# Optimization experiments

Measured on AMD Instinct MI355X. Metric: run time of the kernel, lower is better.

Reference implementation:

```python
import jax, jax.numpy as jnp
import numpy as np


def _forward(f2e_emb, score_mat, rel_features, Wk, bk,
             batch_heads, batch_rels, batch_tails, edge_mat, eps):
    B, N, D = f2e_emb.shape
    R = rel_features.shape[0]
    dt = f2e_emb.dtype
    # -cdist(x, x) then row softmax (F.softmax dim=1 on a 2D mat == last axis)
    x2 = jnp.sum(f2e_emb * f2e_emb, axis=-1)                              # [B,N]
    d2 = x2[:, :, None] + x2[:, None, :] - 2.0 * jnp.einsum('bnd,bmd->bnm', f2e_emb, f2e_emb)
    sim = jax.nn.softmax(-jnp.sqrt(jnp.maximum(d2, 0.0)), axis=-1)        # [B,N,N]
    prob = jnp.einsum('bnk,bmk->bnm', sim, score_mat)                     # sim @ score_mat.T
    cand = (prob > eps) & (edge_mat < 1)                                  # candidate (row,col) pairs
    # torch.multinomial(sim[row], 1) per candidate pair -> gumbel-max categorical,
    # one independent draw per (b, row, col) over the row's similarity distribution
    logits = jnp.log(sim)[:, :, None, :]                                  # [B,N,1,N]
    s = jax.random.categorical(jax.random.key(42),
                               jax.lax.stop_gradient(jnp.broadcast_to(logits, (B, N, N, N))),
                               axis=-1)                                    # [B,N,N]
    b3 = jnp.arange(B)[:, None, None]
    r3 = jnp.arange(N)[None, :, None]
    c3 = jnp.arange(N)[None, None, :]
    new_rel = edge_mat[b3, s, c3]                                          # [B,N,N]
    valid = (cand & (new_rel != 0)).astype(dt)
    # per-(node, relation) incidence counts: exactly equivalent to the
    # fact2head_mat/fact2tail_mat sparse.mm aggregation of kb_self_linear(rel_features[rel])
    counts = jnp.zeros((B * N * R,), dt)
    counts = counts.at[((b3 * N + r3) * R + new_rel).ravel()].add(valid.ravel())  # new edge -> head
    counts = counts.at[((b3 * N + c3) * R + new_rel).ravel()].add(valid.ravel())  # new edge -> tail
    b2 = jnp.arange(B)[:, None]
    ones = jnp.ones(batch_heads.shape, dt)
    counts = counts.at[((b2 * N + batch_heads) * R + batch_rels).ravel()].add(ones.ravel())
    counts = counts.at[((b2 * N + batch_tails) * R + batch_rels).ravel()].add(ones.ravel())
    counts = counts.reshape(B, N, R)
    Wr = rel_features @ Wk + bk                                            # kb_self_linear(rel_features) [R,O]
    return jax.nn.relu(jnp.einsum('bnr,ro->bno', counts, Wr))              # [B,N,O]


def setup_inputs():
    key = jax.random.key(0)
    ks = jax.random.split(key, 10)
    B, N, D, O, R, E = 8, 256, 256, 256, 512, 8192
    return {
        'f2e_emb': jax.random.normal(ks[0], (B, N, D), jnp.float32),
        'score_mat': jax.random.normal(ks[1], (B, N, N), jnp.float32),
        'rel_features': jax.random.normal(ks[2], (R, D), jnp.float32),
        'Wk': jax.random.normal(ks[3], (D, O), jnp.float32) / np.sqrt(D).astype(np.float32),
        'bk': jnp.zeros((O,), jnp.float32),
        'local_entity': jax.random.randint(ks[4], (B, N), 0, N, jnp.int32),
        'batch_heads': jax.random.randint(ks[5], (B, E), 0, N, jnp.int32),
        'batch_rels': jax.random.randint(ks[6], (B, E), 0, R, jnp.int32),
        'batch_tails': jax.random.randint(ks[7], (B, E), 0, N, jnp.int32),
        'edge_mat': jax.random.randint(ks[8], (B, N, N), 0, 4, jnp.int32),
        'eps': 0,
    }


def reference(f2e_emb, score_mat, rel_features, Wk, bk, local_entity,
              batch_heads, batch_rels, batch_tails, edge_mat, eps):
    return _forward(f2e_emb, score_mat, rel_features, Wk, bk,
                    batch_heads, batch_rels, batch_tails, edge_mat, eps)
```

## Files before the change

kernel.cpp:

```cpp
#include <hip/hip_runtime.h>
#include <stdint.h>

#define B 8
#define N 256
#define D 256
#define O 256
#define R 512
#define E 8192
#define TR 4
#define F32_TINY 1.17549435e-38f

__device__ __forceinline__ void threefry2x32_k42(uint32_t x0, uint32_t x1,
                                                 uint32_t& o0, uint32_t& o1) {
  const uint32_t ks0 = 0u;
  const uint32_t ks1 = 42u;
  const uint32_t ks2 = 0u ^ 42u ^ 0x1BD11BDAu;
  x0 += ks0; x1 += ks1;
#define TF_R(r) { x0 += x1; x1 = (x1 << (r)) | (x1 >> (32 - (r))); x1 ^= x0; }
  TF_R(13) TF_R(15) TF_R(26) TF_R(6)
  x0 += ks1; x1 += ks2 + 1u;
  TF_R(17) TF_R(29) TF_R(16) TF_R(24)
  x0 += ks2; x1 += ks0 + 2u;
  TF_R(13) TF_R(15) TF_R(26) TF_R(6)
  x0 += ks0; x1 += ks1 + 3u;
  TF_R(17) TF_R(29) TF_R(16) TF_R(24)
  x0 += ks1; x1 += ks2 + 4u;
  TF_R(13) TF_R(15) TF_R(26) TF_R(6)
  x0 += ks2; x1 += ks0 + 5u;
#undef TF_R
  o0 = x0; o1 = x1;
}

__device__ __forceinline__ float gumbel_from_bits_f(float f) {
  float u = (f == 0.0f) ? F32_TINY : f;
  return -logf(-logf(u));
}

__global__ __launch_bounds__(256) void transpose_kernel(const float* __restrict__ score,
                                                        float* __restrict__ scoreT,
                                                        const float* __restrict__ f2e,
                                                        float* __restrict__ f2eT) {
  __shared__ float tile[64][65];
  int blk = blockIdx.x;
  const float* src = (blk < 128) ? score : f2e;
  float* dst = (blk < 128) ? scoreT : f2eT;
  int b7 = blk & 127;
  int bb = b7 >> 4, t = b7 & 15, ti = t >> 2, tj = t & 3;
  size_t base = (size_t)bb * 65536;
  int c = threadIdx.x & 63, r4 = threadIdx.x >> 6;
#pragma unroll
  for (int rr = 0; rr < 64; rr += 4) {
    int row = rr + r4;
    tile[row][c] = src[base + (size_t)(ti * 64 + row) * 256 + tj * 64 + c];
  }
  __syncthreads();
#pragma unroll
  for (int rr = 0; rr < 64; rr += 4) {
    int row = rr + r4;
    dst[base + (size_t)(tj * 64 + row) * 256 + ti * 64 + c] = tile[c][row];
  }
}

__global__ __launch_bounds__(256) void x2_kernel(const float* __restrict__ f2e,
                                                 float* __restrict__ x2) {
  int i = blockIdx.x * 256 + threadIdx.x;
  const float4* p = (const float4*)(f2e + (size_t)i * D);
  double s = 0.0;
  for (int d = 0; d < D / 4; ++d) {
    float4 v = p[d];
    s += (double)v.x * v.x; s += (double)v.y * v.y;
    s += (double)v.z * v.z; s += (double)v.w * v.w;
  }
  x2[i] = (float)s;
}

__global__ __launch_bounds__(256) void wr_kernel(const float* __restrict__ relf,
                                                 const float* __restrict__ Wk,
                                                 const float* __restrict__ bk,
                                                 float* __restrict__ Wr) {
  int r0 = blockIdx.x * TR;
  int o = threadIdx.x;
  __shared__ float rrow[TR][D];
#pragma unroll
  for (int r = 0; r < TR; ++r) rrow[r][o] = relf[(size_t)(r0 + r) * D + o];
  __syncthreads();
  double acc[TR] = {0, 0, 0, 0};
  for (int d = 0; d < D; d += 4) {
    float w0 = Wk[(size_t)(d + 0) * O + o];
    float w1 = Wk[(size_t)(d + 1) * O + o];
    float w2 = Wk[(size_t)(d + 2) * O + o];
    float w3 = Wk[(size_t)(d + 3) * O + o];
#pragma unroll
    for (int r = 0; r < TR; ++r) {
      float4 a = *(const float4*)&rrow[r][d];
      acc[r] += (double)a.x * w0; acc[r] += (double)a.y * w1;
      acc[r] += (double)a.z * w2; acc[r] += (double)a.w * w3;
    }
  }
  float bv = bk[o];
#pragma unroll
  for (int r = 0; r < TR; ++r) Wr[(size_t)(r0 + r) * O + o] = (float)acc[r] + bv;
}

__global__ __launch_bounds__(256) void sim_kernel(const float* __restrict__ f2e,
                                                  const float* __restrict__ f2eT,
                                                  const float* __restrict__ x2,
                                                  float* __restrict__ sim,
                                                  float* __restrict__ logits,
                                                  float* __restrict__ laux) {
  int bn0 = blockIdx.x * TR;
  int b = bn0 >> 8;
  int tid = threadIdx.x, lane = tid & 63, w = tid >> 6;
  __shared__ float arow[TR][256];
  __shared__ float nbuf[TR][256];
#pragma unroll
  for (int r = 0; r < TR; ++r) arow[r][tid] = f2e[(size_t)(bn0 + r) * 256 + tid];
  __syncthreads();
  double acc[TR] = {0, 0, 0, 0};
  const float* fT = f2eT + (size_t)b * 65536 + tid;
  for (int dd = 0; dd < 256; dd += 4) {
    float b0 = fT[(size_t)(dd + 0) * 256];
    float b1 = fT[(size_t)(dd + 1) * 256];
    float b2 = fT[(size_t)(dd + 2) * 256];
    float b3 = fT[(size_t)(dd + 3) * 256];
#pragma unroll
    for (int r = 0; r < TR; ++r) {
      float4 a = *(const float4*)&arow[r][dd];
      acc[r] += (double)a.x * b0; acc[r] += (double)a.y * b1;
      acc[r] += (double)a.z * b2; acc[r] += (double)a.w * b3;
    }
  }
  float x2c = x2[b * 256 + tid];
#pragma unroll
  for (int r = 0; r < TR; ++r) {
    float d2 = (x2[bn0 + r] + x2c) - 2.0f * (float)acc[r];
    nbuf[r][tid] = -sqrtf(fmaxf(d2, 0.0f));
  }
  __syncthreads();
  float v0 = nbuf[w][lane], v1 = nbuf[w][lane + 64],
        v2 = nbuf[w][lane + 128], v3 = nbuf[w][lane + 192];
  float mx = fmaxf(fmaxf(v0, v1), fmaxf(v2, v3));
#pragma unroll
  for (int off = 32; off > 0; off >>= 1) mx = fmaxf(mx, __shfl_xor(mx, off));
  float p0 = expf(v0 - mx), p1 = expf(v1 - mx), p2 = expf(v2 - mx), p3 = expf(v3 - mx);
  double sd = (double)p0 + (double)p1 + (double)p2 + (double)p3;
#pragma unroll
  for (int off = 32; off > 0; off >>= 1) sd += __shfl_xor(sd, off);
  float denom = (float)sd;
  float s0 = p0 / denom, s1 = p1 / denom, s2 = p2 / denom, s3 = p3 / denom;
  size_t rb = (size_t)(bn0 + w) * 256;
  sim[rb + lane] = s0; sim[rb + lane + 64] = s1;
  sim[rb + lane + 128] = s2; sim[rb + lane + 192] = s3;
  float l0 = logf(s0), l1 = logf(s1), l2 = logf(s2), l3 = logf(s3);
  logits[rb + lane] = l0; logits[rb + lane + 64] = l1;
  logits[rb + lane + 128] = l2; logits[rb + lane + 192] = l3;
  int dm = (bn0 + w) & 255;
  int dj = dm >> 6, dl = dm & 63;
  float e0 = (dj == 0 && lane == dl) ? -3.4e38f : l0;
  float e1 = (dj == 1 && lane == dl) ? -3.4e38f : l1;
  float e2 = (dj == 2 && lane == dl) ? -3.4e38f : l2;
  float e3 = (dj == 3 && lane == dl) ? -3.4e38f : l3;
  float Lm = fmaxf(fmaxf(e0, e1), fmaxf(e2, e3));
#pragma unroll
  for (int off = 32; off > 0; off >>= 1) Lm = fmaxf(Lm, __shfl_xor(Lm, off));
  float lown = (dj == 0) ? l0 : (dj == 1) ? l1 : (dj == 2) ? l2 : l3;
  float l_n = __shfl(lown, dl);
  if (lane == 0) {
    laux[2 * (bn0 + w) + 0] = l_n;
    laux[2 * (bn0 + w) + 1] = Lm;
  }
}

__global__ __launch_bounds__(256) void cand_kernel(const float* __restrict__ sim,
                                                   const float* __restrict__ scoreT,
                                                   const int* __restrict__ edge,
                                                   const int* __restrict__ epsp,
                                                   unsigned char* __restrict__ cand) {
  int bn0 = blockIdx.x * TR;
  int b = bn0 >> 8;
  int tid = threadIdx.x;
  __shared__ float srow[TR][256];
#pragma unroll
  for (int r = 0; r < TR; ++r) srow[r][tid] = sim[(size_t)(bn0 + r) * 256 + tid];
  __syncthreads();
  double acc[TR] = {0, 0, 0, 0};
  const float* sT = scoreT + (size_t)b * 65536 + tid;
  for (int kk = 0; kk < 256; kk += 4) {
    float b0 = sT[(size_t)(kk + 0) * 256];
    float b1 = sT[(size_t)(kk + 1) * 256];
    float b2 = sT[(size_t)(kk + 2) * 256];
    float b3 = sT[(size_t)(kk + 3) * 256];
#pragma unroll
    for (int r = 0; r < TR; ++r) {
      float4 a = *(const float4*)&srow[r][kk];
      acc[r] += (double)a.x * b0; acc[r] += (double)a.y * b1;
      acc[r] += (double)a.z * b2; acc[r] += (double)a.w * b3;
    }
  }
  float epsv = (float)epsp[0];
#pragma unroll
  for (int r = 0; r < TR; ++r) {
    int em = edge[(size_t)(bn0 + r) * 256 + tid];
    cand[(size_t)(bn0 + r) * 256 + tid] =
        ((float)acc[r] > epsv && em < 1) ? 1 : 0;
  }
}

__global__ __launch_bounds__(256) void sample_kernel(const float* __restrict__ logits,
                                                     const float* __restrict__ laux,
                                                     const unsigned char* __restrict__ cand,
                                                     const int* __restrict__ edge,
                                                     float* __restrict__ counts) {
  int wid = threadIdx.x >> 6;
  int lane = threadIdx.x & 63;
  int row = blockIdx.x * 4 + wid;
  if (!cand[row]) return;
  int b = row >> 16;
  int n = (row >> 8) & 255;
  int c = row & 255;
  uint32_t base = (uint32_t)row << 8;
  float u0, u1, u2, u3;
  {
    uint32_t a0, a1;
#define GEN_U(q, dst)                                                     \
    threefry2x32_k42(0u, base + (uint32_t)((q) * 64 + lane), a0, a1);      \
    dst = __uint_as_float((((a0 ^ a1) >> 9)) | 0x3f800000u) - 1.0f;
    GEN_U(0, u0) GEN_U(1, u1) GEN_U(2, u2) GEN_U(3, u3)
#undef GEN_U
  }
  float l_n  = laux[2 * ((b << 8) + n) + 0];
  float Lmax = laux[2 * ((b << 8) + n) + 1];
  int qo = n >> 6;
  float uo = (qo == 0) ? u0 : (qo == 1) ? u1 : (qo == 2) ? u2 : u3;
  float u_n = __shfl(uo, n & 63);
  float v_n = gumbel_from_bits_f(u_n) + l_n;
  float thr_g = (v_n - Lmax) - 0.125f;
  float u_thr = expf(-expf(-thr_g));
  bool owner = (lane == (n & 63));
  bool anyc = ((u0 > u_thr) && !(owner && qo == 0)) |
              ((u1 > u_thr) && !(owner && qo == 1)) |
              ((u2 > u_thr) && !(owner && qo == 2)) |
              ((u3 > u_thr) && !(owner && qo == 3));
  if (!__any(anyc)) return;

  const float* lrow = logits + (size_t)((b << 8) + n) * N;
  float bestv = -1e30f;
  int besti = 0;
  for (int q = 0; q < 4; ++q) {
    int k = q * 64 + lane;
    uint32_t o0, o1;
    threefry2x32_k42(0u, base + (uint32_t)k, o0, o1);
    uint32_t bits = o0 ^ o1;
    float f = __uint_as_float((bits >> 9) | 0x3f800000u) - 1.0f;
    float g = gumbel_from_bits_f(f);
    float v = g + lrow[k];
    if (v > bestv || (v == bestv && k < besti)) { bestv = v; besti = k; }
  }
  for (int off = 32; off > 0; off >>= 1) {
    float ov = __shfl_down(bestv, off);
    int oi = __shfl_down(besti, off);
    if (ov > bestv || (ov == bestv && oi < besti)) { bestv = ov; besti = oi; }
  }
  if (lane == 0) {
    int nr = edge[(size_t)((b << 8) + besti) * N + c];
    if (nr != 0) {
      atomicAdd(&counts[(size_t)((b << 8) + n) * R + nr], 1.0f);
      atomicAdd(&counts[(size_t)((b << 8) + c) * R + nr], 1.0f);
    }
  }
}

__global__ __launch_bounds__(256) void batch_kernel(const int* __restrict__ heads,
                                                    const int* __restrict__ rels,
                                                    const int* __restrict__ tails,
                                                    float* __restrict__ counts) {
  int i = blockIdx.x * 256 + threadIdx.x;
  int b = i >> 13;
  int h = heads[i], r = rels[i], t = tails[i];
  atomicAdd(&counts[(size_t)(b * N + h) * R + r], 1.0f);
  atomicAdd(&counts[(size_t)(b * N + t) * R + r], 1.0f);
}

__global__ __launch_bounds__(256) void out_kernel(const float* __restrict__ counts,
                                                  const float* __restrict__ Wr,
                                                  float* __restrict__ out) {
  int bn0 = blockIdx.x * TR;
  int o = threadIdx.x;
  __shared__ float crow[TR][R];
#pragma unroll
  for (int r = 0; r < TR; ++r) {
    crow[r][o] = counts[(size_t)(bn0 + r) * R + o];
    crow[r][o + 256] = counts[(size_t)(bn0 + r) * R + 256 + o];
  }
  __syncthreads();
  float acc[TR] = {0, 0, 0, 0};
  for (int k = 0; k < R; k += 4) {
    float w0 = Wr[(size_t)(k + 0) * O + o];
    float w1 = Wr[(size_t)(k + 1) * O + o];
    float w2 = Wr[(size_t)(k + 2) * O + o];
    float w3 = Wr[(size_t)(k + 3) * O + o];
#pragma unroll
    for (int r = 0; r < TR; ++r) {
      float4 cv = *(const float4*)&crow[r][k];
      acc[r] += cv.x * w0; acc[r] += cv.y * w1;
      acc[r] += cv.z * w2; acc[r] += cv.w * w3;
    }
  }
#pragma unroll
  for (int r = 0; r < TR; ++r)
    out[(size_t)(bn0 + r) * O + o] = fmaxf(acc[r], 0.0f);
}

extern "C" void kernel_launch(void* const* d_in, const int* in_sizes, int n_in,
                              void* d_out, int out_size, void* d_ws, size_t ws_size,
                              hipStream_t stream) {
  (void)in_sizes; (void)n_in; (void)out_size; (void)ws_size;
  const float* f2e   = (const float*)d_in[0];
  const float* score = (const float*)d_in[1];
  const float* relf  = (const float*)d_in[2];
  const float* Wk    = (const float*)d_in[3];
  const float* bk    = (const float*)d_in[4];
  const int* heads   = (const int*)d_in[6];
  const int* rels    = (const int*)d_in[7];
  const int* tails   = (const int*)d_in[8];
  const int* edge    = (const int*)d_in[9];
  const int* epsp    = (const int*)d_in[10];
  float* out = (float*)d_out;

  float* ws     = (float*)d_ws;
  float* sim    = ws;
  float* logits = sim + 524288;
  float* x2     = logits + 524288;
  float* Wr     = x2 + 2048;
  float* counts = Wr + 131072;
  float* scoreT = counts;
  float* f2eT   = counts + 524288;
  unsigned char* cand = (unsigned char*)(counts + 1048576);
  float* laux   = (float*)(cand + 524288);

  transpose_kernel<<<256, 256, 0, stream>>>(score, scoreT, f2e, f2eT);
  x2_kernel<<<(B * N) / 256, 256, 0, stream>>>(f2e, x2);
  wr_kernel<<<R / TR, 256, 0, stream>>>(relf, Wk, bk, Wr);
  sim_kernel<<<(B * N) / TR, 256, 0, stream>>>(f2e, f2eT, x2, sim, logits, laux);
  cand_kernel<<<(B * N) / TR, 256, 0, stream>>>(sim, scoreT, edge, epsp, cand);
  hipMemsetAsync(counts, 0, (size_t)B * N * R * sizeof(float), stream);
  sample_kernel<<<(B * N * N) / 4, 256, 0, stream>>>(logits, laux, cand, edge, counts);
  batch_kernel<<<(B * E) / 256, 256, 0, stream>>>(heads, rels, tails, counts);
  out_kernel<<<(B * N) / TR, 256, 0, stream>>>(counts, Wr, out);
}
```

Baseline: 171.6 us.

## Fuse prep/sim/cand kernels and compact candidates into worklist for sampling

Merges transpose and Wr projection into one prep kernel, folds x2 computation and the candidate matmul into the sim kernel (keeping sim rows in shared memory instead of writing them out), and replaces the per-pair candidate byte mask with an atomically compacted worklist. The sample kernel then runs a grid-stride loop over only the candidate pairs and also absorbs the batch-edge atomics. The output GEMM tile grows to 8 rows. Worklist order is nondeterministic, but the float count atomics only add 1.0, so the result is unaffected. This removes several launches and the sparse-warp early-exit overhead, at the cost of a global atomic counter.

```diff
diff --git a/kernel.cpp b/kernel.cpp
--- a/kernel.cpp
+++ b/kernel.cpp
@@ -8,6 +8,8 @@
 #define R 512
 #define E 8192
 #define TR 4
+#define TRO 8
+#define NSW 8192
 #define F32_TINY 1.17549435e-38f
 
 __device__ __forceinline__ void threefry2x32_k42(uint32_t x0, uint32_t x1,
@@ -36,93 +38,90 @@
   return -logf(-logf(u));
 }
 
-__global__ __launch_bounds__(256) void transpose_kernel(const float* __restrict__ score,
-                                                        float* __restrict__ scoreT,
-                                                        const float* __restrict__ f2e,
-                                                        float* __restrict__ f2eT) {
-  __shared__ float tile[64][65];
+__global__ __launch_bounds__(256) void prep_kernel(const float* __restrict__ score,
+                                                   float* __restrict__ scoreT,
+                                                   const float* __restrict__ f2e,
+                                                   float* __restrict__ f2eT,
+                                                   const float* __restrict__ relf,
+                                                   const float* __restrict__ Wk,
+                                                   const float* __restrict__ bk,
+                                                   float* __restrict__ Wr,
+                                                   int* __restrict__ wcount) {
   int blk = blockIdx.x;
-  const float* src = (blk < 128) ? score : f2e;
-  float* dst = (blk < 128) ? scoreT : f2eT;
-  int b7 = blk & 127;
-  int bb = b7 >> 4, t = b7 & 15, ti = t >> 2, tj = t & 3;
-  size_t base = (size_t)bb * 65536;
-  int c = threadIdx.x & 63, r4 = threadIdx.x >> 6;
-#pragma unroll
-  for (int rr = 0; rr < 64; rr += 4) {
-    int row = rr + r4;
-    tile[row][c] = src[base + (size_t)(ti * 64 + row) * 256 + tj * 64 + c];
-  }
-  __syncthreads();
-#pragma unroll
-  for (int rr = 0; rr < 64; rr += 4) {
-    int row = rr + r4;
-    dst[base + (size_t)(tj * 64 + row) * 256 + ti * 64 + c] = tile[c][row];
-  }
-}
-
-__global__ __launch_bounds__(256) void x2_kernel(const float* __restrict__ f2e,
-                                                 float* __restrict__ x2) {
-  int i = blockIdx.x * 256 + threadIdx.x;
-  const float4* p = (const float4*)(f2e + (size_t)i * D);
-  double s = 0.0;
-  for (int d = 0; d < D / 4; ++d) {
-    float4 v = p[d];
-    s += (double)v.x * v.x; s += (double)v.y * v.y;
-    s += (double)v.z * v.z; s += (double)v.w * v.w;
-  }
-  x2[i] = (float)s;
-}
-
-__global__ __launch_bounds__(256) void wr_kernel(const float* __restrict__ relf,
-                                                 const float* __restrict__ Wk,
-                                                 const float* __restrict__ bk,
-                                                 float* __restrict__ Wr) {
-  int r0 = blockIdx.x * TR;
-  int o = threadIdx.x;
-  __shared__ float rrow[TR][D];
-#pragma unroll
-  for (int r = 0; r < TR; ++r) rrow[r][o] = relf[(size_t)(r0 + r) * D + o];
-  __syncthreads();
-  double acc[TR] = {0, 0, 0, 0};
-  for (int d = 0; d < D; d += 4) {
-    float w0 = Wk[(size_t)(d + 0) * O + o];
-    float w1 = Wk[(size_t)(d + 1) * O + o];
-    float w2 = Wk[(size_t)(d + 2) * O + o];
-    float w3 = Wk[(size_t)(d + 3) * O + o];
-#pragma unroll
-    for (int r = 0; r < TR; ++r) {
-      float4 a = *(const float4*)&rrow[r][d];
-      acc[r] += (double)a.x * w0; acc[r] += (double)a.y * w1;
-      acc[r] += (double)a.z * w2; acc[r] += (double)a.w * w3;
-    }
-  }
-  float bv = bk[o];
-#pragma unroll
-  for (int r = 0; r < TR; ++r) Wr[(size_t)(r0 + r) * O + o] = (float)acc[r] + bv;
-}
-
-__global__ __launch_bounds__(256) void sim_kernel(const float* __restrict__ f2e,
-                                                  const float* __restrict__ f2eT,
-                                                  const float* __restrict__ x2,
-                                                  float* __restrict__ sim,
-                                                  float* __restrict__ logits,
-                                                  float* __restrict__ laux) {
+  if (blk == 0 && threadIdx.x == 0) *wcount = 0;
+  if (blk < 256) {
+    __shared__ float tile[64][65];
+    const float* src = (blk < 128) ? score : f2e;
+    float* dst = (blk < 128) ? scoreT : f2eT;
+    int b7 = blk & 127;
+    int bb = b7 >> 4, t = b7 & 15, ti = t >> 2, tj = t & 3;
+    size_t base = (size_t)bb * 65536;
+    int c = threadIdx.x & 63, r4 = threadIdx.x >> 6;
+#pragma unroll
+    for (int rr = 0; rr < 64; rr += 4) {
+      int row = rr + r4;
+      tile[row][c] = src[base + (size_t)(ti * 64 + row) * 256 + tj * 64 + c];
+    }
+    __syncthreads();
+#pragma unroll
+    for (int rr = 0; rr < 64; rr += 4) {
+      int row = rr + r4;
+      dst[base + (size_t)(tj * 64 + row) * 256 + ti * 64 + c] = tile[c][row];
+    }
+  } else {
+    __shared__ float rrow[TR][D];
+    int r0 = (blk - 256) * TR;
+    int o = threadIdx.x;
+#pragma unroll
+    for (int r = 0; r < TR; ++r) rrow[r][o] = relf[(size_t)(r0 + r) * D + o];
+    __syncthreads();
+    double acc[TR] = {0, 0, 0, 0};
+    for (int d = 0; d < D; d += 4) {
+      float w0 = Wk[(size_t)(d + 0) * O + o];
+      float w1 = Wk[(size_t)(d + 1) * O + o];
+      float w2 = Wk[(size_t)(d + 2) * O + o];
+      float w3 = Wk[(size_t)(d + 3) * O + o];
+#pragma unroll
+      for (int r = 0; r < TR; ++r) {
+        float4 a = *(const float4*)&rrow[r][d];
+        acc[r] += (double)a.x * w0; acc[r] += (double)a.y * w1;
+        acc[r] += (double)a.z * w2; acc[r] += (double)a.w * w3;
+      }
+    }
+    float bv = bk[o];
+#pragma unroll
+    for (int r = 0; r < TR; ++r) Wr[(size_t)(r0 + r) * O + o] = (float)acc[r] + bv;
+  }
+}
+
+__global__ __launch_bounds__(256) void simcand_kernel(const float* __restrict__ f2e,
+                                                      const float* __restrict__ f2eT,
+                                                      const float* __restrict__ scoreT,
+                                                      const int* __restrict__ edge,
+                                                      const int* __restrict__ epsp,
+                                                      float* __restrict__ logits,
+                                                      float* __restrict__ laux,
+                                                      int* __restrict__ wlist,
+                                                      int* __restrict__ wcount) {
   int bn0 = blockIdx.x * TR;
   int b = bn0 >> 8;
   int tid = threadIdx.x, lane = tid & 63, w = tid >> 6;
   __shared__ float arow[TR][256];
   __shared__ float nbuf[TR][256];
+  __shared__ float x2s[256];
 #pragma unroll
   for (int r = 0; r < TR; ++r) arow[r][tid] = f2e[(size_t)(bn0 + r) * 256 + tid];
   __syncthreads();
   double acc[TR] = {0, 0, 0, 0};
+  double ax2 = 0.0;
   const float* fT = f2eT + (size_t)b * 65536 + tid;
   for (int dd = 0; dd < 256; dd += 4) {
     float b0 = fT[(size_t)(dd + 0) * 256];
     float b1 = fT[(size_t)(dd + 1) * 256];
     float b2 = fT[(size_t)(dd + 2) * 256];
     float b3 = fT[(size_t)(dd + 3) * 256];
+    ax2 += (double)b0 * b0; ax2 += (double)b1 * b1;
+    ax2 += (double)b2 * b2; ax2 += (double)b3 * b3;
 #pragma unroll
     for (int r = 0; r < TR; ++r) {
       float4 a = *(const float4*)&arow[r][dd];
@@ -130,60 +129,52 @@
       acc[r] += (double)a.z * b2; acc[r] += (double)a.w * b3;
     }
   }
-  float x2c = x2[b * 256 + tid];
+  float x2c = (float)ax2;
+  x2s[tid] = x2c;
+  __syncthreads();
 #pragma unroll
   for (int r = 0; r < TR; ++r) {
-    float d2 = (x2[bn0 + r] + x2c) - 2.0f * (float)acc[r];
+    float x2r = x2s[(bn0 + r) & 255];
+    float d2 = (x2r + x2c) - 2.0f * (float)acc[r];
     nbuf[r][tid] = -sqrtf(fmaxf(d2, 0.0f));
   }
   __syncthreads();
-  float v0 = nbuf[w][lane], v1 = nbuf[w][lane + 64],
-        v2 = nbuf[w][lane + 128], v3 = nbuf[w][lane + 192];
-  float mx = fmaxf(fmaxf(v0, v1), fmaxf(v2, v3));
-#pragma unroll
-  for (int off = 32; off > 0; off >>= 1) mx = fmaxf(mx, __shfl_xor(mx, off));
-  float p0 = expf(v0 - mx), p1 = expf(v1 - mx), p2 = expf(v2 - mx), p3 = expf(v3 - mx);
-  double sd = (double)p0 + (double)p1 + (double)p2 + (double)p3;
-#pragma unroll
-  for (int off = 32; off > 0; off >>= 1) sd += __shfl_xor(sd, off);
-  float denom = (float)sd;
-  float s0 = p0 / denom, s1 = p1 / denom, s2 = p2 / denom, s3 = p3 / denom;
-  size_t rb = (size_t)(bn0 + w) * 256;
-  sim[rb + lane] = s0; sim[rb + lane + 64] = s1;
-  sim[rb + lane + 128] = s2; sim[rb + lane + 192] = s3;
-  float l0 = logf(s0), l1 = logf(s1), l2 = logf(s2), l3 = logf(s3);
-  logits[rb + lane] = l0; logits[rb + lane + 64] = l1;
-  logits[rb + lane + 128] = l2; logits[rb + lane + 192] = l3;
-  int dm = (bn0 + w) & 255;
-  int dj = dm >> 6, dl = dm & 63;
-  float e0 = (dj == 0 && lane == dl) ? -3.4e38f : l0;
-  float e1 = (dj == 1 && lane == dl) ? -3.4e38f : l1;
-  float e2 = (dj == 2 && lane == dl) ? -3.4e38f : l2;
-  float e3 = (dj == 3 && lane == dl) ? -3.4e38f : l3;
-  float Lm = fmaxf(fmaxf(e0, e1), fmaxf(e2, e3));
-#pragma unroll
-  for (int off = 32; off > 0; off >>= 1) Lm = fmaxf(Lm, __shfl_xor(Lm, off));
-  float lown = (dj == 0) ? l0 : (dj == 1) ? l1 : (dj == 2) ? l2 : l3;
-  float l_n = __shfl(lown, dl);
-  if (lane == 0) {
-    laux[2 * (bn0 + w) + 0] = l_n;
-    laux[2 * (bn0 + w) + 1] = Lm;
-  }
-}
-
-__global__ __launch_bounds__(256) void cand_kernel(const float* __restrict__ sim,
-                                                   const float* __restrict__ scoreT,
-                                                   const int* __restrict__ edge,
-                                                   const int* __restrict__ epsp,
-                                                   unsigned char* __restrict__ cand) {
-  int bn0 = blockIdx.x * TR;
-  int b = bn0 >> 8;
-  int tid = threadIdx.x;
-  __shared__ float srow[TR][256];
-#pragma unroll
-  for (int r = 0; r < TR; ++r) srow[r][tid] = sim[(size_t)(bn0 + r) * 256 + tid];
-  __syncthreads();
-  double acc[TR] = {0, 0, 0, 0};
+  {
+    float v0 = nbuf[w][lane], v1 = nbuf[w][lane + 64],
+          v2 = nbuf[w][lane + 128], v3 = nbuf[w][lane + 192];
+    float mx = fmaxf(fmaxf(v0, v1), fmaxf(v2, v3));
+#pragma unroll
+    for (int off = 32; off > 0; off >>= 1) mx = fmaxf(mx, __shfl_xor(mx, off));
+    float p0 = expf(v0 - mx), p1 = expf(v1 - mx), p2 = expf(v2 - mx), p3 = expf(v3 - mx);
+    double sd = (double)p0 + (double)p1 + (double)p2 + (double)p3;
+#pragma unroll
+    for (int off = 32; off > 0; off >>= 1) sd += __shfl_xor(sd, off);
+    float denom = (float)sd;
+    float s0 = p0 / denom, s1 = p1 / denom, s2 = p2 / denom, s3 = p3 / denom;
+    arow[w][lane] = s0; arow[w][lane + 64] = s1;
+    arow[w][lane + 128] = s2; arow[w][lane + 192] = s3;
+    float l0 = logf(s0), l1 = logf(s1), l2 = logf(s2), l3 = logf(s3);
+    size_t rb = (size_t)(bn0 + w) * 256;
+    logits[rb + lane] = l0; logits[rb + lane + 64] = l1;
+    logits[rb + lane + 128] = l2; logits[rb + lane + 192] = l3;
+    int dm = (bn0 + w) & 255;
+    int dj = dm >> 6, dl = dm & 63;
+    float e0 = (dj == 0 && lane == dl) ? -3.4e38f : l0;
+    float e1 = (dj == 1 && lane == dl) ? -3.4e38f : l1;
+    float e2 = (dj == 2 && lane == dl) ? -3.4e38f : l2;
+    float e3 = (dj == 3 && lane == dl) ? -3.4e38f : l3;
+    float Lm = fmaxf(fmaxf(e0, e1), fmaxf(e2, e3));
+#pragma unroll
+    for (int off = 32; off > 0; off >>= 1) Lm = fmaxf(Lm, __shfl_xor(Lm, off));
+    float lown = (dj == 0) ? l0 : (dj == 1) ? l1 : (dj == 2) ? l2 : l3;
+    float l_n = __shfl(lown, dl);
+    if (lane == 0) {
+      laux[2 * (bn0 + w) + 0] = l_n;
+      laux[2 * (bn0 + w) + 1] = Lm;
+    }
+  }
+  __syncthreads();
+  double acc2[TR] = {0, 0, 0, 0};
   const float* sT = scoreT + (size_t)b * 65536 + tid;
   for (int kk = 0; kk < 256; kk += 4) {
     float b0 = sT[(size_t)(kk + 0) * 256];
@@ -192,122 +183,135 @@
     float b3 = sT[(size_t)(kk + 3) * 256];
 #pragma unroll
     for (int r = 0; r < TR; ++r) {
-      float4 a = *(const float4*)&srow[r][kk];
-      acc[r] += (double)a.x * b0; acc[r] += (double)a.y * b1;
-      acc[r] += (double)a.z * b2; acc[r] += (double)a.w * b3;
+      float4 a = *(const float4*)&arow[r][kk];
+      acc2[r] += (double)a.x * b0; acc2[r] += (double)a.y * b1;
+      acc2[r] += (double)a.z * b2; acc2[r] += (double)a.w * b3;
     }
   }
   float epsv = (float)epsp[0];
 #pragma unroll
   for (int r = 0; r < TR; ++r) {
-    int em = edge[(size_t)(bn0 + r) * 256 + tid];
-    cand[(size_t)(bn0 + r) * 256 + tid] =
-        ((float)acc[r] > epsv && em < 1) ? 1 : 0;
+    int row = (bn0 + r) * 256 + tid;
+    int em = edge[(size_t)row];
+    bool active = ((float)acc2[r] > epsv) && (em < 1);
+    unsigned long long mask = __ballot(active);
+    int cnt = __popcll(mask);
+    int basev = 0;
+    if (lane == 0 && cnt) basev = atomicAdd(wcount, cnt);
+    basev = __shfl(basev, 0);
+    if (active) {
+      int pos = basev + __popcll(mask & ((1ull << lane) - 1ull));
+      wlist[pos] = row;
+    }
   }
 }
 
 __global__ __launch_bounds__(256) void sample_kernel(const float* __restrict__ logits,
                                                      const float* __restrict__ laux,
-                                                     const unsigned char* __restrict__ cand,
+                                                     const int* __restrict__ wlist,
+                                                     const int* __restrict__ wcount,
                                                      const int* __restrict__ edge,
+                                                     const int* __restrict__ heads,
+                                                     const int* __restrict__ rels,
+                                                     const int* __restrict__ tails,
                                                      float* __restrict__ counts) {
-  int wid = threadIdx.x >> 6;
+  int blk = blockIdx.x;
+  if (blk >= 2048) {
+    int i = (blk - 2048) * 256 + threadIdx.x;
+    int b = i >> 13;
+    int h = heads[i], r = rels[i], t = tails[i];
+    atomicAdd(&counts[(size_t)(b * N + h) * R + r], 1.0f);
+    atomicAdd(&counts[(size_t)(b * N + t) * R + r], 1.0f);
+    return;
+  }
   int lane = threadIdx.x & 63;
-  int row = blockIdx.x * 4 + wid;
-  if (!cand[row]) return;
-  int b = row >> 16;
-  int n = (row >> 8) & 255;
-  int c = row & 255;
-  uint32_t base = (uint32_t)row << 8;
-  float u0, u1, u2, u3;
-  {
-    uint32_t a0, a1;
+  int gw = blk * 4 + (threadIdx.x >> 6);
+  int cnt = *wcount;
+  for (int idx = gw; idx < cnt; idx += NSW) {
+    int row = wlist[idx];
+    int b = row >> 16;
+    int n = (row >> 8) & 255;
+    int c = row & 255;
+    uint32_t base = (uint32_t)row << 8;
+    float u0, u1, u2, u3;
+    {
+      uint32_t a0, a1;
 #define GEN_U(q, dst)                                                     \
-    threefry2x32_k42(0u, base + (uint32_t)((q) * 64 + lane), a0, a1);      \
-    dst = __uint_as_float((((a0 ^ a1) >> 9)) | 0x3f800000u) - 1.0f;
-    GEN_U(0, u0) GEN_U(1, u1) GEN_U(2, u2) GEN_U(3, u3)
+      threefry2x32_k42(0u, base + (uint32_t)((q) * 64 + lane), a0, a1);    \
+      dst = __uint_as_float((((a0 ^ a1) >> 9)) | 0x3f800000u) - 1.0f;
+      GEN_U(0, u0) GEN_U(1, u1) GEN_U(2, u2) GEN_U(3, u3)
 #undef GEN_U
-  }
-  float l_n  = laux[2 * ((b << 8) + n) + 0];
-  float Lmax = laux[2 * ((b << 8) + n) + 1];
-  int qo = n >> 6;
-  float uo = (qo == 0) ? u0 : (qo == 1) ? u1 : (qo == 2) ? u2 : u3;
-  float u_n = __shfl(uo, n & 63);
-  float v_n = gumbel_from_bits_f(u_n) + l_n;
-  float thr_g = (v_n - Lmax) - 0.125f;
-  float u_thr = expf(-expf(-thr_g));
-  bool owner = (lane == (n & 63));
-  bool anyc = ((u0 > u_thr) && !(owner && qo == 0)) |
-              ((u1 > u_thr) && !(owner && qo == 1)) |
-              ((u2 > u_thr) && !(owner && qo == 2)) |
-              ((u3 > u_thr) && !(owner && qo == 3));
-  if (!__any(anyc)) return;
-
-  const float* lrow = logits + (size_t)((b << 8) + n) * N;
-  float bestv = -1e30f;
-  int besti = 0;
-  for (int q = 0; q < 4; ++q) {
-    int k = q * 64 + lane;
-    uint32_t o0, o1;
-    threefry2x32_k42(0u, base + (uint32_t)k, o0, o1);
-    uint32_t bits = o0 ^ o1;
-    float f = __uint_as_float((bits >> 9) | 0x3f800000u) - 1.0f;
-    float g = gumbel_from_bits_f(f);
-    float v = g + lrow[k];
-    if (v > bestv || (v == bestv && k < besti)) { bestv = v; besti = k; }
-  }
-  for (int off = 32; off > 0; off >>= 1) {
-    float ov = __shfl_down(bestv, off);
-    int oi = __shfl_down(besti, off);
-    if (ov > bestv || (ov == bestv && oi < besti)) { bestv = ov; besti = oi; }
-  }
-  if (lane == 0) {
-    int nr = edge[(size_t)((b << 8) + besti) * N + c];
-    if (nr != 0) {
-      atomicAdd(&counts[(size_t)((b << 8) + n) * R + nr], 1.0f);
-      atomicAdd(&counts[(size_t)((b << 8) + c) * R + nr], 1.0f);
-    }
-  }
-}
-
-__global__ __launch_bounds__(256) void batch_kernel(const int* __restrict__ heads,
-                                                    const int* __restrict__ rels,
-                                                    const int* __restrict__ tails,
-                                                    float* __restrict__ counts) {
-  int i = blockIdx.x * 256 + threadIdx.x;
-  int b = i >> 13;
-  int h = heads[i], r = rels[i], t = tails[i];
-  atomicAdd(&counts[(size_t)(b * N + h) * R + r], 1.0f);
-  atomicAdd(&counts[(size_t)(b * N + t) * R + r], 1.0f);
+    }
+    float l_n  = laux[2 * ((b << 8) + n) + 0];
+    float Lmax = laux[2 * ((b << 8) + n) + 1];
+    int qo = n >> 6;
+    float uo = (qo == 0) ? u0 : (qo == 1) ? u1 : (qo == 2) ? u2 : u3;
+    float u_n = __shfl(uo, n & 63);
+    float v_n = gumbel_from_bits_f(u_n) + l_n;
+    float thr_g = (v_n - Lmax) - 0.125f;
+    float u_thr = expf(-expf(-thr_g));
+    bool owner = (lane == (n & 63));
+    bool anyc = ((u0 > u_thr) && !(owner && qo == 0)) |
+                ((u1 > u_thr) && !(owner && qo == 1)) |
+                ((u2 > u_thr) && !(owner && qo == 2)) |
+                ((u3 > u_thr) && !(owner && qo == 3));
+    if (!__any(anyc)) continue;
+
+    const float* lrow = logits + (size_t)((b << 8) + n) * N;
+    float bestv = -1e30f;
+    int besti = 0;
+    for (int q = 0; q < 4; ++q) {
+      int k = q * 64 + lane;
+      uint32_t o0, o1;
+      threefry2x32_k42(0u, base + (uint32_t)k, o0, o1);
+      uint32_t bits = o0 ^ o1;
+      float f = __uint_as_float((bits >> 9) | 0x3f800000u) - 1.0f;
+      float g = gumbel_from_bits_f(f);
+      float v = g + lrow[k];
+      if (v > bestv || (v == bestv && k < besti)) { bestv = v; besti = k; }
+    }
+    for (int off = 32; off > 0; off >>= 1) {
+      float ov = __shfl_down(bestv, off);
+      int oi = __shfl_down(besti, off);
+      if (ov > bestv || (ov == bestv && oi < besti)) { bestv = ov; besti = oi; }
+    }
+    if (lane == 0) {
+      int nr = edge[(size_t)((b << 8) + besti) * N + c];
+      if (nr != 0) {
+        atomicAdd(&counts[(size_t)((b << 8) + n) * R + nr], 1.0f);
+        atomicAdd(&counts[(size_t)((b << 8) + c) * R + nr], 1.0f);
+      }
+    }
+  }
 }
 
 __global__ __launch_bounds__(256) void out_kernel(const float* __restrict__ counts,
                                                   const float* __restrict__ Wr,
                                                   float* __restrict__ out) {
-  int bn0 = blockIdx.x * TR;
+  int bn0 = blockIdx.x * TRO;
   int o = threadIdx.x;
-  __shared__ float crow[TR][R];
-#pragma unroll
-  for (int r = 0; r < TR; ++r) {
+  __shared__ float crow[TRO][R];
+#pragma unroll
+  for (int r = 0; r < TRO; ++r) {
     crow[r][o] = counts[(size_t)(bn0 + r) * R + o];
     crow[r][o + 256] = counts[(size_t)(bn0 + r) * R + 256 + o];
   }
   __syncthreads();
-  float acc[TR] = {0, 0, 0, 0};
+  float acc[TRO] = {0, 0, 0, 0, 0, 0, 0, 0};
   for (int k = 0; k < R; k += 4) {
     float w0 = Wr[(size_t)(k + 0) * O + o];
     float w1 = Wr[(size_t)(k + 1) * O + o];
     float w2 = Wr[(size_t)(k + 2) * O + o];
     float w3 = Wr[(size_t)(k + 3) * O + o];
 #pragma unroll
-    for (int r = 0; r < TR; ++r) {
+    for (int r = 0; r < TRO; ++r) {
       float4 cv = *(const float4*)&crow[r][k];
       acc[r] += cv.x * w0; acc[r] += cv.y * w1;
       acc[r] += cv.z * w2; acc[r] += cv.w * w3;
     }
   }
 #pragma unroll
-  for (int r = 0; r < TR; ++r)
+  for (int r = 0; r < TRO; ++r)
     out[(size_t)(bn0 + r) * O + o] = fmaxf(acc[r], 0.0f);
 }
 
@@ -328,23 +332,21 @@
   float* out = (float*)d_out;
 
   float* ws     = (float*)d_ws;
-  float* sim    = ws;
-  float* logits = sim + 524288;
-  float* x2     = logits + 524288;
-  float* Wr     = x2 + 2048;
+  float* logits = ws;
+  float* Wr     = logits + 524288;
   float* counts = Wr + 131072;
   float* scoreT = counts;
   float* f2eT   = counts + 524288;
-  unsigned char* cand = (unsigned char*)(counts + 1048576);
-  float* laux   = (float*)(cand + 524288);
-
-  transpose_kernel<<<256, 256, 0, stream>>>(score, scoreT, f2e, f2eT);
-  x2_kernel<<<(B * N) / 256, 256, 0, stream>>>(f2e, x2);
-  wr_kernel<<<R / TR, 256, 0, stream>>>(relf, Wk, bk, Wr);
-  sim_kernel<<<(B * N) / TR, 256, 0, stream>>>(f2e, f2eT, x2, sim, logits, laux);
-  cand_kernel<<<(B * N) / TR, 256, 0, stream>>>(sim, scoreT, edge, epsp, cand);
+  float* laux   = counts + 1048576;
+  int*   wlist  = (int*)(laux + 4096);
+  int*   wcount = wlist + 524288;
+
+  prep_kernel<<<384, 256, 0, stream>>>(score, scoreT, f2e, f2eT,
+                                       relf, Wk, bk, Wr, wcount);
+  simcand_kernel<<<(B * N) / TR, 256, 0, stream>>>(f2e, f2eT, scoreT, edge, epsp,
+                                                   logits, laux, wlist, wcount);
   hipMemsetAsync(counts, 0, (size_t)B * N * R * sizeof(float), stream);
-  sample_kernel<<<(B * N * N) / 4, 256, 0, stream>>>(logits, laux, cand, edge, counts);
-  batch_kernel<<<(B * E) / 256, 256, 0, stream>>>(heads, rels, tails, counts);
-  out_kernel<<<(B * N) / TR, 256, 0, stream>>>(counts, Wr, out);
-}
+  sample_kernel<<<2048 + 256, 256, 0, stream>>>(logits, laux, wlist, wcount, edge,
+                                                heads, rels, tails, counts);
+  out_kernel<<<(B * N) / TRO, 256, 0, stream>>>(counts, Wr, out);
+}
```

Measured after the change: 214.1 us. 1.25x slower.
